# Performance work log

Measured on AMD Instinct MI355X. Metric: run time of the kernel, lower is better.

## Reference

```python
import jax, jax.numpy as jnp
import numpy as np

N = 50000
E = 800000
IN_DIM = 768
HID = 128
OUT = 128
R = 8


def rgcn_conv(x, edge_index, edge_type, weight, root, bias, num_relations):
    # PyG RGCNConv (aggr='mean'): per-relation transform of source nodes,
    # mean-aggregated at destination per relation, plus root transform + bias.
    n = x.shape[0]
    src, dst = edge_index[0], edge_index[1]
    # [R, N, out]: transform every node by every relation weight (R is small)
    h_all = jnp.einsum('ni,rio->rno', x, weight)
    msg = h_all[edge_type, src]  # [E, out] gathered per-edge message
    # per-(dst, relation) mean normalization
    seg = dst * num_relations + edge_type
    counts = jax.ops.segment_sum(jnp.ones((src.shape[0],), dtype=x.dtype), seg,
                                 num_segments=n * num_relations)
    norm = 1.0 / jnp.maximum(counts[seg], 1.0)
    agg = jax.ops.segment_sum(msg * norm[:, None], dst, num_segments=n)
    return agg + x @ root + bias


def setup_inputs() -> dict:
    key = jax.random.key(0)
    ks = jax.random.split(key, 9)
    feature = jax.random.normal(ks[0], (N, IN_DIM), dtype=jnp.float32)
    edge_index = jax.random.randint(ks[1], (2, E), 0, N, dtype=jnp.int64 if jax.config.jax_enable_x64 else jnp.int32)
    edge_type = jax.random.randint(ks[2], (E,), 0, R, dtype=edge_index.dtype)
    s1 = 1.0 / np.sqrt(IN_DIM)
    s2 = 1.0 / np.sqrt(HID)
    w1 = jax.random.uniform(ks[3], (R, IN_DIM, HID), jnp.float32, -s1, s1)
    root1 = jax.random.uniform(ks[4], (IN_DIM, HID), jnp.float32, -s1, s1)
    b1 = jnp.zeros((HID,), jnp.float32)
    w2 = jax.random.uniform(ks[5], (R, HID, OUT), jnp.float32, -s2, s2)
    root2 = jax.random.uniform(ks[6], (HID, OUT), jnp.float32, -s2, s2)
    b2 = jnp.zeros((OUT,), jnp.float32)
    return {"feature": feature, "edge_index": edge_index, "edge_type": edge_type,
            "w1": w1, "root1": root1, "b1": b1, "w2": w2, "root2": root2, "b2": b2}


def reference(feature, edge_index, edge_type, w1, root1, b1, w2, root2, b2):
    x = rgcn_conv(feature, edge_index, edge_type, w1, root1, b1, R)
    x = jax.nn.relu(x)
    # dropout(p=0.5) is identity in eval mode
    x = rgcn_conv(x, edge_index, edge_type, w2, root2, b2, R)
    return jnp.concatenate((feature, x), axis=1)
```

## Files before the change

### kernel.cpp

```cpp
#include <hip/hip_runtime.h>
#include <hip/hip_bf16.h>


typedef __hip_bfloat16 bf16;
typedef __attribute__((ext_vector_type(4))) float f32x4;
typedef __attribute__((ext_vector_type(8))) short s16x8;

#define IN_DIM 768
#define NREL   8
#define NTL    9
#define LDH    (NTL*128)

__device__ __forceinline__ float bf2f(unsigned short u) {
    return __uint_as_float((unsigned)u << 16);
}
__device__ __forceinline__ unsigned short f2bf(float f) {
    __hip_bfloat16 b = __float2bfloat16(f);
    return *(unsigned short*)&b;
}

__device__ __forceinline__ void gload16(const void* g, void* l) {
    __builtin_amdgcn_global_load_lds(
        (const __attribute__((address_space(1))) void*)g,
        (__attribute__((address_space(3))) void*)l, 16, 0, 0);
}

__global__ __launch_bounds__(256) void mfma_gemm(
    const bf16* __restrict__ A, int lda, const bf16* __restrict__ BT,
    bf16* __restrict__ C, int K, int nmt, int ntl)
{
    __shared__ bf16 Asm[128 * 64];
    __shared__ bf16 Bsm[128 * 64];

    const int tid  = threadIdx.x;
    const int lane = tid & 63;
    const int wrow = ((tid >> 7) & 1) * 64;
    const int wcol = ((tid >> 6) & 1) * 64;

    const int nwg  = nmt * ntl;
    const int orig = blockIdx.x;
    const int xcd  = orig & 7;
    const int q    = nwg >> 3, rr = nwg & 7;
    const int bse  = (xcd < rr) ? xcd * (q + 1) : rr * (q + 1) + (xcd - rr) * q;
    const int w    = bse + (orig >> 3);
    const int ntile = w % ntl;
    const int mtile = w / ntl;
    const long m0   = (long)mtile * 128;
    const bf16* Bp  = BT + (long)ntile * 128 * K;
    const int  ldh  = ntl * 128;
    const int  ncol0 = ntile * 128;

    f32x4 acc[4][4];
#pragma unroll
    for (int i = 0; i < 4; ++i)
#pragma unroll
        for (int j = 0; j < 4; ++j) acc[i][j] = (f32x4){0.f, 0.f, 0.f, 0.f};

    for (int k0 = 0; k0 < K; k0 += 64) {
#pragma unroll
        for (int i = 0; i < 4; ++i) {
            const int flat = i * 256 + tid;
            const int row  = flat >> 3;
            const int sch  = (flat & 7) ^ (row & 7);
            char* ldsA = (char*)Asm + (i * 256 + (tid & 192)) * 16;
            char* ldsB = (char*)Bsm + (i * 256 + (tid & 192)) * 16;
            gload16(A  + (m0 + row) * (long)lda + k0 + sch * 8, ldsA);
            gload16(Bp + (long)row * K          + k0 + sch * 8, ldsB);
        }
        __syncthreads();

#pragma unroll
        for (int ks = 0; ks < 2; ++ks) {
            s16x8 af[4], bfr[4];
            const int g = ks * 4 + (lane >> 4);
#pragma unroll
            for (int i = 0; i < 4; ++i) {
                const int ar = wrow + i * 16 + (lane & 15);
                af[i] = *(const s16x8*)((const char*)Asm + ar * 128 +
                                        (g ^ (ar & 7)) * 16);
                const int br = wcol + i * 16 + (lane & 15);
                bfr[i] = *(const s16x8*)((const char*)Bsm + br * 128 +
                                         (g ^ (br & 7)) * 16);
            }
#pragma unroll
            for (int i = 0; i < 4; ++i)
#pragma unroll
                for (int j = 0; j < 4; ++j)
                    acc[i][j] = __builtin_amdgcn_mfma_f32_16x16x32_bf16(
                        af[i], bfr[j], acc[i][j], 0, 0, 0);
        }
        __syncthreads();
    }

#pragma unroll
    for (int i = 0; i < 4; ++i) {
#pragma unroll
        for (int r = 0; r < 4; ++r) {
            const long row = m0 + wrow + i * 16 + (lane >> 4) * 4 + r;
#pragma unroll
            for (int j = 0; j < 4; ++j) {
                const int col = wcol + j * 16 + (lane & 15);
                C[row * (long)ldh + ncol0 + col] =
                    __float2bfloat16(acc[i][j][r]);
            }
        }
    }
}

__global__ __launch_bounds__(256) void rgcn_count(
    const int* __restrict__ edst, const int* __restrict__ etype, int E,
    float* __restrict__ counts)
{
    const int e = blockIdx.x * blockDim.x + threadIdx.x;
    if (e < E) atomicAdd(&counts[(long)edst[e] * NREL + etype[e]], 1.0f);
}

__global__ __launch_bounds__(256) void deg_block_scan(
    const float* __restrict__ counts, int N, int* __restrict__ rowstart,
    int* __restrict__ partials)
{
    __shared__ int s[256];
    const int d = blockIdx.x * 256 + threadIdx.x;
    int deg = 0;
    if (d < N) {
#pragma unroll
        for (int t = 0; t < NREL; ++t) deg += (int)counts[(long)d * NREL + t];
    }
    s[threadIdx.x] = deg;
    __syncthreads();
    for (int off = 1; off < 256; off <<= 1) {
        int v = (threadIdx.x >= off) ? s[threadIdx.x - off] : 0;
        __syncthreads();
        s[threadIdx.x] += v;
        __syncthreads();
    }
    if (d < N) rowstart[d] = s[threadIdx.x] - deg;
    if (threadIdx.x == 255) partials[blockIdx.x] = s[255];
}

__global__ __launch_bounds__(256) void scan_partials(int* partials, int nb)
{
    __shared__ int s[256];
    const int v = (threadIdx.x < nb) ? partials[threadIdx.x] : 0;
    s[threadIdx.x] = v;
    __syncthreads();
    for (int off = 1; off < 256; off <<= 1) {
        int u = (threadIdx.x >= off) ? s[threadIdx.x - off] : 0;
        __syncthreads();
        s[threadIdx.x] += u;
        __syncthreads();
    }
    if (threadIdx.x < nb) partials[threadIdx.x] = s[threadIdx.x] - v;
}

__global__ __launch_bounds__(256) void add_base(
    int* __restrict__ rowstart, const int* __restrict__ partials, int N, int E)
{
    const int d = blockIdx.x * 256 + threadIdx.x;
    if (d < N) rowstart[d] += partials[blockIdx.x];
    if (d == 0) rowstart[N] = E;
}

__global__ __launch_bounds__(256) void csr_fill(
    const int* __restrict__ esrc, const int* __restrict__ edst,
    const int* __restrict__ etype, int E, const int* __restrict__ rowstart,
    int* __restrict__ cursor, int* __restrict__ epack)
{
    const int e = blockIdx.x * 256 + threadIdx.x;
    if (e >= E) return;
    const int d = edst[e];
    const int pos = atomicAdd(&cursor[d], 1);
    epack[rowstart[d] + pos] = esrc[e] | (etype[e] << 24);
}

__global__ __launch_bounds__(256) void rgcn_gather(
    const int* __restrict__ rowstart, const int* __restrict__ epack,
    const float* __restrict__ counts, const bf16* __restrict__ h,
    bf16* __restrict__ agg, int N, int NP)
{
    const int wid  = (blockIdx.x * 256 + threadIdx.x) >> 6;
    if (wid >= NP) return;
    const int lane = threadIdx.x & 63;
    const int half = lane >> 5;
    const int l32  = lane & 31;
    float a0 = 0.f, a1 = 0.f, a2 = 0.f, a3 = 0.f;
    if (wid < N) {
        const int start = rowstart[wid];
        const int end   = rowstart[wid + 1];
        const float nrm =
            1.0f / fmaxf(counts[(long)wid * NREL + (lane & 7)], 1.0f);
        for (int base = start; base < end; base += 64) {
            const int rem = end - base;
            const int cnt = rem < 64 ? rem : 64;
            int wv = 0;
            if (lane < cnt) wv = epack[base + lane];
            for (int i = 0; i < cnt; i += 2) {
                const int  idx   = i + half;
                const bool valid = idx < cnt;
                const int  word  = __shfl(wv, idx);
                int src = 0, t = 0;
                if (valid) { src = word & 0xFFFFFF; t = ((unsigned)word) >> 24; }
                const float norm = __shfl(nrm, t);
                if (valid) {
                    const ushort4 raw = *(const ushort4*)(
                        h + (long)src * LDH + t * 128 + l32 * 4);
                    a0 += bf2f(raw.x) * norm;
                    a1 += bf2f(raw.y) * norm;
                    a2 += bf2f(raw.z) * norm;
                    a3 += bf2f(raw.w) * norm;
                }
            }
        }
    }
    a0 += __shfl(a0, lane ^ 32);
    a1 += __shfl(a1, lane ^ 32);
    a2 += __shfl(a2, lane ^ 32);
    a3 += __shfl(a3, lane ^ 32);
    if (half == 0) {
        ushort4 o;
        o.x = f2bf(a0); o.y = f2bf(a1); o.z = f2bf(a2); o.w = f2bf(a3);
        *(ushort4*)(agg + (long)wid * 128 + l32 * 4) = o;
    }
}

__global__ __launch_bounds__(256) void epilogue1(
    const bf16* __restrict__ h, const bf16* __restrict__ agg,
    const float* __restrict__ b1, bf16* __restrict__ x1b, int NP)
{
    const int idx = blockIdx.x * 256 + threadIdx.x;
    if (idx >= NP * 16) return;
    const int n  = idx >> 4;
    const int c8 = (idx & 15) << 3;
    const s16x8 hv = *(const s16x8*)(h + (long)n * LDH + NREL * 128 + c8);
    const s16x8 av = *(const s16x8*)(agg + (long)n * 128 + c8);
    const float4 bA = *(const float4*)(b1 + c8);
    const float4 bB = *(const float4*)(b1 + c8 + 4);
    const float bb[8] = {bA.x, bA.y, bA.z, bA.w, bB.x, bB.y, bB.z, bB.w};
    bf16 o[8];
#pragma unroll
    for (int j = 0; j < 8; ++j) {
        float v = bf2f((unsigned short)hv[j]) +
                  bf2f((unsigned short)av[j]) + bb[j];
        o[j] = __float2bfloat16(fmaxf(v, 0.f));
    }
    *(s16x8*)(x1b + (long)n * 128 + c8) = *(const s16x8*)o;
}

__global__ __launch_bounds__(256) void epilogue2(
    const bf16* __restrict__ h, const bf16* __restrict__ agg,
    const float* __restrict__ b2, float* __restrict__ out, int N)
{
    const int idx = blockIdx.x * 256 + threadIdx.x;
    if (idx >= N * 16) return;
    const int n  = idx >> 4;
    const int c8 = (idx & 15) << 3;
    const s16x8 hv = *(const s16x8*)(h + (long)n * LDH + NREL * 128 + c8);
    const s16x8 av = *(const s16x8*)(agg + (long)n * 128 + c8);
    const float4 bA = *(const float4*)(b2 + c8);
    const float4 bB = *(const float4*)(b2 + c8 + 4);
    const float bb[8] = {bA.x, bA.y, bA.z, bA.w, bB.x, bB.y, bB.z, bB.w};
    float v[8];
#pragma unroll
    for (int j = 0; j < 8; ++j)
        v[j] = bf2f((unsigned short)hv[j]) + bf2f((unsigned short)av[j]) + bb[j];
    float* op = out + (long)n * (IN_DIM + 128) + IN_DIM + c8;
    *(float4*)op       = make_float4(v[0], v[1], v[2], v[3]);
    *(float4*)(op + 4) = make_float4(v[4], v[5], v[6], v[7]);
}

__global__ __launch_bounds__(256) void cvt_copy(
    const float* __restrict__ f, bf16* __restrict__ fb,
    float* __restrict__ out, int N)
{
    const int idx = blockIdx.x * 256 + threadIdx.x;
    if (idx >= N * (IN_DIM / 8)) return;
    const int n  = idx / (IN_DIM / 8);
    const int k8 = (idx % (IN_DIM / 8)) << 3;
    const float4 a = *(const float4*)(f + (long)n * IN_DIM + k8);
    const float4 b = *(const float4*)(f + (long)n * IN_DIM + k8 + 4);
    float* op = out + (long)n * (IN_DIM + 128) + k8;
    *(float4*)op       = a;
    *(float4*)(op + 4) = b;
    bf16 o[8];
    o[0] = __float2bfloat16(a.x); o[1] = __float2bfloat16(a.y);
    o[2] = __float2bfloat16(a.z); o[3] = __float2bfloat16(a.w);
    o[4] = __float2bfloat16(b.x); o[5] = __float2bfloat16(b.y);
    o[6] = __float2bfloat16(b.z); o[7] = __float2bfloat16(b.w);
    *(s16x8*)(fb + (long)n * IN_DIM + k8) = *(const s16x8*)o;
}

__global__ __launch_bounds__(256) void cvt_w_transpose(
    const float* __restrict__ w, bf16* __restrict__ wt, int K, long total)
{
    const long idx = (long)blockIdx.x * 256 + threadIdx.x;
    if (idx >= total) return;
    const int  k  = (int)(idx % K);
    const long rn = idx / K;
    const int  n  = (int)(rn & 127);
    const long r  = rn >> 7;
    wt[idx] = __float2bfloat16(w[(r * K + k) * 128 + n]);
}

extern "C" void kernel_launch(void* const* d_in, const int* in_sizes, int n_in,
                              void* d_out, int out_size, void* d_ws,
                              size_t ws_size, hipStream_t stream)
{
    const float* feature = (const float*)d_in[0];
    const int*   eidx    = (const int*)d_in[1];
    const int*   etype   = (const int*)d_in[2];
    const float* w1      = (const float*)d_in[3];
    const float* root1   = (const float*)d_in[4];
    const float* b1      = (const float*)d_in[5];
    const float* w2      = (const float*)d_in[6];
    const float* root2   = (const float*)d_in[7];
    const float* b2      = (const float*)d_in[8];

    const int N = in_sizes[0] / IN_DIM;
    const int E = in_sizes[2];
    const int* esrc = eidx;
    const int* edst = eidx + E;
    const int NMT = (N + 127) / 128;
    const int NP  = NMT * 128;

    char* p = (char*)d_ws;
    auto carve = [&](size_t b) { char* q = p; p += (b + 255) & ~(size_t)255; return q; };
    float* counts   = (float*)carve((size_t)N * NREL * 4);
    bf16*  agg      = (bf16*)carve((size_t)NP * 128 * 2);
    bf16*  x1b      = (bf16*)carve((size_t)NP * 128 * 2);
    bf16*  fb       = (bf16*)carve((size_t)NP * IN_DIM * 2);
    bf16*  w1m      = (bf16*)carve((size_t)NTL * 128 * IN_DIM * 2);
    bf16*  w2m      = (bf16*)carve((size_t)NTL * 128 * 128 * 2);
    int*   rowstart = (int*)carve((size_t)(N + 1) * 4);
    int*   cursor   = (int*)carve((size_t)N * 4);
    int*   partials = (int*)carve(1024);
    int*   epack    = (int*)carve((size_t)E * 4);
    bf16*  h        = (bf16*)carve((size_t)NP * LDH * 2);
    (void)ws_size;

    const int count_blks = (E + 255) / 256;
    const int nblk       = (N + 255) / 256;
    const int gat_blks   = NP / 4;
    const int gemm_blks  = NMT * NTL;

    cvt_copy<<<(N * (IN_DIM / 8) + 255) / 256, 256, 0, stream>>>(
        feature, fb, (float*)d_out, N);
    {
        long t1 = (long)NREL * 128 * IN_DIM;
        cvt_w_transpose<<<(int)((t1 + 255) / 256), 256, 0, stream>>>(
            w1, w1m, IN_DIM, t1);
        long t1r = (long)128 * IN_DIM;
        cvt_w_transpose<<<(int)((t1r + 255) / 256), 256, 0, stream>>>(
            root1, w1m + (long)NREL * 128 * IN_DIM, IN_DIM, t1r);
        long t2 = (long)NREL * 128 * 128;
        cvt_w_transpose<<<(int)((t2 + 255) / 256), 256, 0, stream>>>(
            w2, w2m, 128, t2);
        long t2r = (long)128 * 128;
        cvt_w_transpose<<<(int)((t2r + 255) / 256), 256, 0, stream>>>(
            root2, w2m + (long)NREL * 128 * 128, 128, t2r);
    }

    hipMemsetAsync(counts, 0, (size_t)N * NREL * 4, stream);
    rgcn_count<<<count_blks, 256, 0, stream>>>(edst, etype, E, counts);
    deg_block_scan<<<nblk, 256, 0, stream>>>(counts, N, rowstart, partials);
    scan_partials<<<1, 256, 0, stream>>>(partials, nblk);
    add_base<<<nblk, 256, 0, stream>>>(rowstart, partials, N, E);
    hipMemsetAsync(cursor, 0, (size_t)N * 4, stream);
    csr_fill<<<count_blks, 256, 0, stream>>>(esrc, edst, etype, E,
                                             rowstart, cursor, epack);

    mfma_gemm<<<gemm_blks, 256, 0, stream>>>(fb, IN_DIM, w1m, h,
                                             IN_DIM, NMT, NTL);
    rgcn_gather<<<gat_blks, 256, 0, stream>>>(rowstart, epack, counts, h,
                                              agg, N, NP);
    epilogue1<<<NP / 16, 256, 0, stream>>>(h, agg, b1, x1b, NP);

    mfma_gemm<<<gemm_blks, 256, 0, stream>>>(x1b, 128, w2m, h,
                                             128, NMT, NTL);
    rgcn_gather<<<gat_blks, 256, 0, stream>>>(rowstart, epack, counts, h,
                                              agg, N, NP);
    epilogue2<<<(N * 16 + 255) / 256, 256, 0, stream>>>(h, agg, b2,
                                                        (float*)d_out, N);
}
```

Measured before the change: 436.9 us.

## Reorder layer-2 as aggregate-then-transform with a single fused concat GEMM

New measurement: 441.2 us. Within noise of the previous version (+1.0%).

```diff
diff --git a/kernel.cpp b/kernel.cpp
--- a/kernel.cpp
+++ b/kernel.cpp
@@ -107,6 +107,88 @@
     }
 }
 
+__global__ __launch_bounds__(256) void gemm_out(
+    const bf16* __restrict__ A, const bf16* __restrict__ BT,
+    const float* __restrict__ bias, float* __restrict__ out,
+    int M, int K, int nmt)
+{
+    __shared__ bf16 Asm[128 * 64];
+    __shared__ bf16 Bsm[128 * 64];
+
+    const int tid  = threadIdx.x;
+    const int lane = tid & 63;
+    const int wrow = ((tid >> 7) & 1) * 64;
+    const int wcol = ((tid >> 6) & 1) * 64;
+
+    const int nwg  = nmt;
+    const int orig = blockIdx.x;
+    const int xcd  = orig & 7;
+    const int q    = nwg >> 3, rr = nwg & 7;
+    const int bse  = (xcd < rr) ? xcd * (q + 1) : rr * (q + 1) + (xcd - rr) * q;
+    const int mtile = bse + (orig >> 3);
+    const long m0   = (long)mtile * 128;
+
+    f32x4 acc[4][4];
+#pragma unroll
+    for (int i = 0; i < 4; ++i)
+#pragma unroll
+        for (int j = 0; j < 4; ++j) acc[i][j] = (f32x4){0.f, 0.f, 0.f, 0.f};
+
+    for (int k0 = 0; k0 < K; k0 += 64) {
+#pragma unroll
+        for (int i = 0; i < 4; ++i) {
+            const int flat = i * 256 + tid;
+            const int row  = flat >> 3;
+            const int sch  = (flat & 7) ^ (row & 7);
+            char* ldsA = (char*)Asm + (i * 256 + (tid & 192)) * 16;
+            char* ldsB = (char*)Bsm + (i * 256 + (tid & 192)) * 16;
+            gload16(A  + (m0 + row) * (long)K + k0 + sch * 8, ldsA);
+            gload16(BT + (long)row * K        + k0 + sch * 8, ldsB);
+        }
+        __syncthreads();
+
+#pragma unroll
+        for (int ks = 0; ks < 2; ++ks) {
+            s16x8 af[4], bfr[4];
+            const int g = ks * 4 + (lane >> 4);
+#pragma unroll
+            for (int i = 0; i < 4; ++i) {
+                const int ar = wrow + i * 16 + (lane & 15);
+                af[i] = *(const s16x8*)((const char*)Asm + ar * 128 +
+                                        (g ^ (ar & 7)) * 16);
+                const int br = wcol + i * 16 + (lane & 15);
+                bfr[i] = *(const s16x8*)((const char*)Bsm + br * 128 +
+                                         (g ^ (br & 7)) * 16);
+            }
+#pragma unroll
+            for (int i = 0; i < 4; ++i)
+#pragma unroll
+                for (int j = 0; j < 4; ++j)
+                    acc[i][j] = __builtin_amdgcn_mfma_f32_16x16x32_bf16(
+                        af[i], bfr[j], acc[i][j], 0, 0, 0);
+        }
+        __syncthreads();
+    }
+
+    float breg[4];
+#pragma unroll
+    for (int j = 0; j < 4; ++j) breg[j] = bias[wcol + j * 16 + (lane & 15)];
+#pragma unroll
+    for (int i = 0; i < 4; ++i) {
+#pragma unroll
+        for (int r = 0; r < 4; ++r) {
+            const long row = m0 + wrow + i * 16 + (lane >> 4) * 4 + r;
+            if (row >= M) continue;
+#pragma unroll
+            for (int j = 0; j < 4; ++j) {
+                const int col = wcol + j * 16 + (lane & 15);
+                out[row * (long)(IN_DIM + 128) + IN_DIM + col] =
+                    acc[i][j][r] + breg[j];
+            }
+        }
+    }
+}
+
 __global__ __launch_bounds__(256) void rgcn_count(
     const int* __restrict__ edst, const int* __restrict__ etype, int E,
     float* __restrict__ counts)
@@ -173,42 +255,40 @@
     epack[rowstart[d] + pos] = esrc[e] | (etype[e] << 24);
 }
 
-__global__ __launch_bounds__(256) void rgcn_gather(
+__global__ __launch_bounds__(256) void rgcn_gather_h(
     const int* __restrict__ rowstart, const int* __restrict__ epack,
-    const float* __restrict__ counts, const bf16* __restrict__ h,
-    bf16* __restrict__ agg, int N, int NP)
+    const float* __restrict__ counts, bf16* __restrict__ h,
+    const float* __restrict__ b1, int N)
 {
     const int wid  = (blockIdx.x * 256 + threadIdx.x) >> 6;
-    if (wid >= NP) return;
+    if (wid >= N) return;
     const int lane = threadIdx.x & 63;
     const int half = lane >> 5;
     const int l32  = lane & 31;
     float a0 = 0.f, a1 = 0.f, a2 = 0.f, a3 = 0.f;
-    if (wid < N) {
-        const int start = rowstart[wid];
-        const int end   = rowstart[wid + 1];
-        const float nrm =
-            1.0f / fmaxf(counts[(long)wid * NREL + (lane & 7)], 1.0f);
-        for (int base = start; base < end; base += 64) {
-            const int rem = end - base;
-            const int cnt = rem < 64 ? rem : 64;
-            int wv = 0;
-            if (lane < cnt) wv = epack[base + lane];
-            for (int i = 0; i < cnt; i += 2) {
-                const int  idx   = i + half;
-                const bool valid = idx < cnt;
-                const int  word  = __shfl(wv, idx);
-                int src = 0, t = 0;
-                if (valid) { src = word & 0xFFFFFF; t = ((unsigned)word) >> 24; }
-                const float norm = __shfl(nrm, t);
-                if (valid) {
-                    const ushort4 raw = *(const ushort4*)(
-                        h + (long)src * LDH + t * 128 + l32 * 4);
-                    a0 += bf2f(raw.x) * norm;
-                    a1 += bf2f(raw.y) * norm;
-                    a2 += bf2f(raw.z) * norm;
-                    a3 += bf2f(raw.w) * norm;
-                }
+    const int start = rowstart[wid];
+    const int end   = rowstart[wid + 1];
+    const float nrm =
+        1.0f / fmaxf(counts[(long)wid * NREL + (lane & 7)], 1.0f);
+    for (int base = start; base < end; base += 64) {
+        const int rem = end - base;
+        const int cnt = rem < 64 ? rem : 64;
+        int wv = 0;
+        if (lane < cnt) wv = epack[base + lane];
+        for (int i = 0; i < cnt; i += 2) {
+            const int  idx   = i + half;
+            const bool valid = idx < cnt;
+            const int  word  = __shfl(wv, idx);
+            int src = 0, t = 0;
+            if (valid) { src = word & 0xFFFFFF; t = ((unsigned)word) >> 24; }
+            const float norm = __shfl(nrm, t);
+            if (valid) {
+                const ushort4 raw = *(const ushort4*)(
+                    h + (long)src * LDH + t * 128 + l32 * 4);
+                a0 += bf2f(raw.x) * norm;
+                a1 += bf2f(raw.y) * norm;
+                a2 += bf2f(raw.z) * norm;
+                a3 += bf2f(raw.w) * norm;
             }
         }
     }
@@ -217,55 +297,65 @@
     a2 += __shfl(a2, lane ^ 32);
     a3 += __shfl(a3, lane ^ 32);
     if (half == 0) {
+        bf16* rp = h + (long)wid * LDH + NREL * 128 + l32 * 4;
+        const ushort4 rt = *(const ushort4*)rp;
+        const float4  bb = *(const float4*)(b1 + l32 * 4);
         ushort4 o;
-        o.x = f2bf(a0); o.y = f2bf(a1); o.z = f2bf(a2); o.w = f2bf(a3);
-        *(ushort4*)(agg + (long)wid * 128 + l32 * 4) = o;
-    }
-}
-
-__global__ __launch_bounds__(256) void epilogue1(
-    const bf16* __restrict__ h, const bf16* __restrict__ agg,
-    const float* __restrict__ b1, bf16* __restrict__ x1b, int NP)
-{
-    const int idx = blockIdx.x * 256 + threadIdx.x;
-    if (idx >= NP * 16) return;
-    const int n  = idx >> 4;
-    const int c8 = (idx & 15) << 3;
-    const s16x8 hv = *(const s16x8*)(h + (long)n * LDH + NREL * 128 + c8);
-    const s16x8 av = *(const s16x8*)(agg + (long)n * 128 + c8);
-    const float4 bA = *(const float4*)(b1 + c8);
-    const float4 bB = *(const float4*)(b1 + c8 + 4);
-    const float bb[8] = {bA.x, bA.y, bA.z, bA.w, bB.x, bB.y, bB.z, bB.w};
-    bf16 o[8];
-#pragma unroll
-    for (int j = 0; j < 8; ++j) {
-        float v = bf2f((unsigned short)hv[j]) +
-                  bf2f((unsigned short)av[j]) + bb[j];
-        o[j] = __float2bfloat16(fmaxf(v, 0.f));
-    }
-    *(s16x8*)(x1b + (long)n * 128 + c8) = *(const s16x8*)o;
-}
-
-__global__ __launch_bounds__(256) void epilogue2(
-    const bf16* __restrict__ h, const bf16* __restrict__ agg,
-    const float* __restrict__ b2, float* __restrict__ out, int N)
-{
-    const int idx = blockIdx.x * 256 + threadIdx.x;
-    if (idx >= N * 16) return;
-    const int n  = idx >> 4;
-    const int c8 = (idx & 15) << 3;
-    const s16x8 hv = *(const s16x8*)(h + (long)n * LDH + NREL * 128 + c8);
-    const s16x8 av = *(const s16x8*)(agg + (long)n * 128 + c8);
-    const float4 bA = *(const float4*)(b2 + c8);
-    const float4 bB = *(const float4*)(b2 + c8 + 4);
-    const float bb[8] = {bA.x, bA.y, bA.z, bA.w, bB.x, bB.y, bB.z, bB.w};
-    float v[8];
-#pragma unroll
-    for (int j = 0; j < 8; ++j)
-        v[j] = bf2f((unsigned short)hv[j]) + bf2f((unsigned short)av[j]) + bb[j];
-    float* op = out + (long)n * (IN_DIM + 128) + IN_DIM + c8;
-    *(float4*)op       = make_float4(v[0], v[1], v[2], v[3]);
-    *(float4*)(op + 4) = make_float4(v[4], v[5], v[6], v[7]);
+        o.x = f2bf(fmaxf(a0 + bf2f(rt.x) + bb.x, 0.f));
+        o.y = f2bf(fmaxf(a1 + bf2f(rt.y) + bb.y, 0.f));
+        o.z = f2bf(fmaxf(a2 + bf2f(rt.z) + bb.z, 0.f));
+        o.w = f2bf(fmaxf(a3 + bf2f(rt.w) + bb.w, 0.f));
+        *(ushort4*)rp = o;
+    }
+}
+
+__global__ __launch_bounds__(256) void rgcn_gather_x(
+    const int* __restrict__ rowstart, const int* __restrict__ epack,
+    const float* __restrict__ counts, bf16* __restrict__ xcat, int N)
+{
+    const int wid  = (blockIdx.x * 256 + threadIdx.x) >> 6;
+    if (wid >= N) return;
+    const int lane = threadIdx.x & 63;
+    float ax[8], ay[8];
+#pragma unroll
+    for (int t = 0; t < 8; ++t) { ax[t] = 0.f; ay[t] = 0.f; }
+    const float nrm =
+        1.0f / fmaxf(counts[(long)wid * NREL + (lane & 7)], 1.0f);
+    const int start = rowstart[wid];
+    const int end   = rowstart[wid + 1];
+    const bf16* x1 = xcat + NREL * 128;
+    for (int base = start; base < end; base += 64) {
+        const int rem = end - base;
+        const int cnt = rem < 64 ? rem : 64;
+        int wv = 0;
+        if (lane < cnt) wv = epack[base + lane];
+        for (int i = 0; i < cnt; ++i) {
+            const int word = __builtin_amdgcn_readfirstlane(__shfl(wv, i));
+            const int src  = word & 0xFFFFFF;
+            const int t    = ((unsigned)word) >> 24;
+            const ushort2 raw =
+                *(const ushort2*)(x1 + (long)src * LDH + (lane << 1));
+            const float vx = bf2f(raw.x), vy = bf2f(raw.y);
+            switch (t) {
+                case 0: ax[0] += vx; ay[0] += vy; break;
+                case 1: ax[1] += vx; ay[1] += vy; break;
+                case 2: ax[2] += vx; ay[2] += vy; break;
+                case 3: ax[3] += vx; ay[3] += vy; break;
+                case 4: ax[4] += vx; ay[4] += vy; break;
+                case 5: ax[5] += vx; ay[5] += vy; break;
+                case 6: ax[6] += vx; ay[6] += vy; break;
+                default: ax[7] += vx; ay[7] += vy; break;
+            }
+        }
+    }
+#pragma unroll
+    for (int t = 0; t < 8; ++t) {
+        const float sc = __shfl(nrm, t);
+        ushort2 o;
+        o.x = f2bf(ax[t] * sc);
+        o.y = f2bf(ay[t] * sc);
+        *(ushort2*)(xcat + (long)wid * LDH + t * 128 + (lane << 1)) = o;
+    }
 }
 
 __global__ __launch_bounds__(256) void cvt_copy(
@@ -301,6 +391,24 @@
     wt[idx] = __float2bfloat16(w[(r * K + k) * 128 + n]);
 }
 
+__global__ __launch_bounds__(256) void cvt_wcat(
+    const float* __restrict__ w2, const float* __restrict__ root2,
+    bf16* __restrict__ wcat)
+{
+    const int idx = blockIdx.x * 256 + threadIdx.x;
+    if (idx >= 128 * LDH) return;
+    const int o = idx / LDH;
+    const int k = idx % LDH;
+    float v;
+    if (k < NREL * 128) {
+        const int t = k >> 7, c = k & 127;
+        v = w2[((long)(t * 128 + c)) * 128 + o];
+    } else {
+        v = root2[(long)(k - NREL * 128) * 128 + o];
+    }
+    wcat[idx] = __float2bfloat16(v);
+}
+
 extern "C" void kernel_launch(void* const* d_in, const int* in_sizes, int n_in,
                               void* d_out, int out_size, void* d_ws,
                               size_t ws_size, hipStream_t stream)
@@ -325,11 +433,9 @@
     char* p = (char*)d_ws;
     auto carve = [&](size_t b) { char* q = p; p += (b + 255) & ~(size_t)255; return q; };
     float* counts   = (float*)carve((size_t)N * NREL * 4);
-    bf16*  agg      = (bf16*)carve((size_t)NP * 128 * 2);
-    bf16*  x1b      = (bf16*)carve((size_t)NP * 128 * 2);
     bf16*  fb       = (bf16*)carve((size_t)NP * IN_DIM * 2);
     bf16*  w1m      = (bf16*)carve((size_t)NTL * 128 * IN_DIM * 2);
-    bf16*  w2m      = (bf16*)carve((size_t)NTL * 128 * 128 * 2);
+    bf16*  wcat     = (bf16*)carve((size_t)128 * LDH * 2);
     int*   rowstart = (int*)carve((size_t)(N + 1) * 4);
     int*   cursor   = (int*)carve((size_t)N * 4);
     int*   partials = (int*)carve(1024);
@@ -339,7 +445,7 @@
 
     const int count_blks = (E + 255) / 256;
     const int nblk       = (N + 255) / 256;
-    const int gat_blks   = NP / 4;
+    const int gat_blks   = (N * 64 + 255) / 256;
     const int gemm_blks  = NMT * NTL;
 
     cvt_copy<<<(N * (IN_DIM / 8) + 255) / 256, 256, 0, stream>>>(
@@ -351,12 +457,7 @@
         long t1r = (long)128 * IN_DIM;
         cvt_w_transpose<<<(int)((t1r + 255) / 256), 256, 0, stream>>>(
             root1, w1m + (long)NREL * 128 * IN_DIM, IN_DIM, t1r);
-        long t2 = (long)NREL * 128 * 128;
-        cvt_w_transpose<<<(int)((t2 + 255) / 256), 256, 0, stream>>>(
-            w2, w2m, 128, t2);
-        long t2r = (long)128 * 128;
-        cvt_w_transpose<<<(int)((t2r + 255) / 256), 256, 0, stream>>>(
-            root2, w2m + (long)NREL * 128 * 128, 128, t2r);
+        cvt_wcat<<<(128 * LDH + 255) / 256, 256, 0, stream>>>(w2, root2, wcat);
     }
 
     hipMemsetAsync(counts, 0, (size_t)N * NREL * 4, stream);
@@ -370,14 +471,11 @@
 
     mfma_gemm<<<gemm_blks, 256, 0, stream>>>(fb, IN_DIM, w1m, h,
                                              IN_DIM, NMT, NTL);
-    rgcn_gather<<<gat_blks, 256, 0, stream>>>(rowstart, epack, counts, h,
-                                              agg, N, NP);
-    epilogue1<<<NP / 16, 256, 0, stream>>>(h, agg, b1, x1b, NP);
-
-    mfma_gemm<<<gemm_blks, 256, 0, stream>>>(x1b, 128, w2m, h,
-                                             128, NMT, NTL);
-    rgcn_gather<<<gat_blks, 256, 0, stream>>>(rowstart, epack, counts, h,
-                                              agg, N, NP);
-    epilogue2<<<(N * 16 + 255) / 256, 256, 0, stream>>>(h, agg, b2,
-                                                        (float*)d_out, N);
-}
+    rgcn_gather_h<<<gat_blks, 256, 0, stream>>>(rowstart, epack, counts,
+                                                h, b1, N);
+
+    rgcn_gather_x<<<gat_blks, 256, 0, stream>>>(rowstart, epack, counts,
+                                                h, N);
+    gemm_out<<<NMT, 256, 0, stream>>>(h, wcat, b2, (float*)d_out, N,
+                                      LDH, NMT);
+}
```
